# Performance work log

Measured on AMD Instinct MI355X. Metric: run time of the kernel, lower is better.

The kernel has to match this reference:

```python
import jax, jax.numpy as jnp
import numpy as np

B, S, D_IN, D_OUT, R = 8, 2048, 2048, 2048, 16

def setup_inputs() -> dict:
    key = jax.random.key(0)
    k = jax.random.split(key, 5)
    scale_w = 1.0 / np.sqrt(D_IN)
    return {
        "x": jax.random.normal(k[0], (B, S, D_IN), dtype=jnp.float32),
        "A_params": jax.random.normal(k[1], (B, D_OUT, R), dtype=jnp.float32) * 0.02,
        "B_params": jax.random.normal(k[2], (B, R, D_IN), dtype=jnp.float32) * 0.02,
        "W": jax.random.normal(k[3], (D_OUT, D_IN), dtype=jnp.float32) * scale_w,
        "b": jax.random.normal(k[4], (D_OUT,), dtype=jnp.float32) * scale_w,
    }

def reference(x, A_params, B_params, W, b):
    # base: x @ W^T + b  -> [B, S, out]
    base_out = jnp.einsum("bsi,oi->bso", x, W) + b
    # intermediate = x @ B^T -> [B, S, r]
    intermediate = jnp.einsum("bsi,bri->bsr", x, B_params)
    # adaptation = intermediate @ A^T -> [B, S, out]
    adaptation = jnp.einsum("bsr,bor->bso", intermediate, A_params)
    return base_out + adaptation
```

## Files before the change

### kernel.cpp

```cpp
#include <hip/hip_runtime.h>
#include <cstdint>
#include <cstddef>

typedef __attribute__((ext_vector_type(4))) float  floatx4;
typedef __attribute__((ext_vector_type(8))) __bf16 bf16x8;
typedef __attribute__((ext_vector_type(8))) unsigned short u16x8;

#define M_TOT 16384
#define N_TOT 2048
#define K_TOT 2048
#define NBATCH 8
#define RLORA 16
#define NT 32

__device__ __forceinline__ unsigned short f32_to_bf16(float f) {
  unsigned u = __float_as_uint(f);
  u += 0x7fffu + ((u >> 16) & 1u);
  return (unsigned short)(u >> 16);
}

__device__ __forceinline__ u16x8 cvt8(const float4& a, const float4& b) {
  u16x8 o;
  o[0] = f32_to_bf16(a.x); o[1] = f32_to_bf16(a.y);
  o[2] = f32_to_bf16(a.z); o[3] = f32_to_bf16(a.w);
  o[4] = f32_to_bf16(b.x); o[5] = f32_to_bf16(b.y);
  o[6] = f32_to_bf16(b.z); o[7] = f32_to_bf16(b.w);
  return o;
}

#define GLOAD_LDS16(gp, lp)                                                        \
  __builtin_amdgcn_global_load_lds((__attribute__((address_space(1))) void*)(void*)(gp), \
                                   (__attribute__((address_space(3))) void*)(void*)(lp), \
                                   16, 0, 0)

template<int V> struct IC { static constexpr int value = V; };

__global__ void k_convert_small(const float* __restrict__ W, const float* __restrict__ Ap,
                                unsigned short* __restrict__ wbf, unsigned short* __restrict__ abf) {
  int b = blockIdx.x;
  if (b < 2048) {
    int i = b * 256 + threadIdx.x;
    const float4* p = (const float4*)W + (size_t)i * 2;
    *(u16x8*)(wbf + (size_t)i * 8) = cvt8(p[0], p[1]);
  } else {
    int row = (b - 2048) * 256 + threadIdx.x;
    const float4* p = (const float4*)(Ap + (size_t)row * RLORA);
    u16x8 lo = cvt8(p[0], p[1]), hi2 = cvt8(p[2], p[3]), z = {0,0,0,0,0,0,0,0};
    u16x8* dst = (u16x8*)(abf + (size_t)row * 32);
    dst[0] = lo; dst[1] = hi2; dst[2] = z; dst[3] = z;
  }
}

__global__ __launch_bounds__(256) void k_xinter(const float* __restrict__ x,
                                                const float* __restrict__ Bp,
                                                unsigned short* __restrict__ xbf,
                                                unsigned short* __restrict__ interbf) {
  const int tid  = threadIdx.x;
  const int lane = tid & 63;
  const int wv   = tid >> 6;
  const int l15  = lane & 15;
  const int hi   = lane >> 4;
  const int m0   = blockIdx.x * 16;
  const int bb   = m0 >> 11;

  floatx4 acc = {0.f, 0.f, 0.f, 0.f};
  const float* bpb = Bp + (size_t)bb * (RLORA * K_TOT);
  const size_t xrow = (size_t)(m0 + l15) * K_TOT;
  const size_t brow = (size_t)l15 * K_TOT;
  const int kb0 = wv * 512;
  for (int kb = kb0; kb < kb0 + 512; kb += 32) {
    const float* xp = x + xrow + kb + hi * 8;
    u16x8 ao = cvt8(*(const float4*)xp, *(const float4*)(xp + 4));
    *(u16x8*)(xbf + xrow + kb + hi * 8) = ao;
    const float* bpp = bpb + brow + kb + hi * 8;
    u16x8 bo = cvt8(*(const float4*)bpp, *(const float4*)(bpp + 4));
    acc = __builtin_amdgcn_mfma_f32_16x16x32_bf16(*(bf16x8*)&ao, *(bf16x8*)&bo, acc, 0, 0, 0);
  }

  __shared__ floatx4 red[4][64];
  red[wv][lane] = acc;
  __syncthreads();
  if (wv == 0) {
    floatx4 s = red[0][lane] + red[1][lane] + red[2][lane] + red[3][lane];
    #pragma unroll
    for (int j = 0; j < 4; ++j) {
      int m = m0 + hi * 4 + j;
      interbf[(size_t)m * 32 + l15] = f32_to_bf16(s[j]);
      interbf[(size_t)m * 32 + 16 + l15] = 0;
    }
  }
}

#define STAGE_A(bufi, h, tt) do {                                                      \
  GLOAD_LDS16(Ag + (h)*262144 + (tt)*64 + gOff0, AsB + ((bufi)*2+(h))*16384 + ldsB0);  \
  GLOAD_LDS16(Ag + (h)*262144 + (tt)*64 + gOff1, AsB + ((bufi)*2+(h))*16384 + ldsB1);  \
} while(0)
#define STAGE_B(bufi, h, tt) do {                                                      \
  GLOAD_LDS16(Bg + (h)*262144 + (tt)*64 + gOff0, BsB + ((bufi)*2+(h))*16384 + ldsB0);  \
  GLOAD_LDS16(Bg + (h)*262144 + (tt)*64 + gOff1, BsB + ((bufi)*2+(h))*16384 + ldsB1);  \
} while(0)
#define RDA_(B2, q, mi, ks) (*(const bf16x8*)(AsB + (B2)*32768 + aBase + (q)*4096 + (mi)*2048 + koff[ks]))
#define RDB_(B2, ni, ks)    (*(const bf16x8*)(BsB + (B2)*32768 + bBase + (ni)*2048 + koff[ks]))
#define BAR() __builtin_amdgcn_s_barrier()

__global__ __launch_bounds__(512, 2) void k_gemm(const unsigned short* __restrict__ xbf,
                                                 const unsigned short* __restrict__ wbf,
                                                 const unsigned short* __restrict__ interbf,
                                                 const unsigned short* __restrict__ abf,
                                                 const float* __restrict__ bias,
                                                 float* __restrict__ out) {
  __shared__ unsigned short As[2][2][8192];
  __shared__ unsigned short Bs[2][2][8192];
  const int tid  = threadIdx.x;
  const int lane = tid & 63;
  const int wid  = tid >> 6;
  const int wm   = wid >> 2;
  const int wn   = wid & 3;
  const int l15  = lane & 15;
  const int hi   = lane >> 4;
  const int swz  = l15 & 7;

  int bid  = blockIdx.x;
  int swzb = ((bid & 7) << 6) | (bid >> 3);
  const int mt = swzb >> 3;
  const int nt = swzb & 7;
  const int mrow0 = mt << 8;
  const int ncol0 = nt << 8;
  const int bb = mrow0 >> 11;

  const int m0 = mrow0 + wm * 128;
  const int n0 = ncol0 + wn * 64;

  const unsigned short* Ag = xbf + (size_t)mrow0 * K_TOT;
  const unsigned short* Bg = wbf + (size_t)ncol0 * K_TOT;
  char* AsB = (char*)As;
  char* BsB = (char*)Bs;

  const int r0    = tid >> 3;
  const int k80   = (tid & 7) ^ (r0 & 7);
  const int gOff0 = r0 * K_TOT + k80 * 8;
  const int gOff1 = gOff0 + 64 * K_TOT;
  const int ldsB0 = wid * 1024;
  const int ldsB1 = 8192 + wid * 1024;

  const int aBase = wm * 16384 + l15 * 128;
  const int bBase = (wn >> 1) * 16384 + (wn & 1) * 8192 + l15 * 128;
  int koff[2];
  koff[0] = ((0 * 4 + hi) ^ swz) * 16;
  koff[1] = ((1 * 4 + hi) ^ swz) * 16;

  floatx4 acc[8][4];
  bf16x8 bfr[4][2];
  bf16x8 af[2][2];

  {
    bf16x8 la[8], lb[4];
    #pragma unroll
    for (int mi = 0; mi < 8; ++mi)
      la[mi] = *(const bf16x8*)(interbf + (size_t)(m0 + mi * 16 + l15) * 32 + hi * 8);
    #pragma unroll
    for (int ni = 0; ni < 4; ++ni)
      lb[ni] = *(const bf16x8*)(abf + ((size_t)bb * N_TOT + n0 + ni * 16 + l15) * 32 + hi * 8);

    STAGE_A(0, 0, 0); STAGE_A(0, 1, 0); STAGE_B(0, 0, 0); STAGE_B(0, 1, 0);
    STAGE_B(1, 0, 1); STAGE_B(1, 1, 1);

    floatx4 z = {0.f, 0.f, 0.f, 0.f};
    #pragma unroll
    for (int mi = 0; mi < 8; ++mi)
      #pragma unroll
      for (int ni = 0; ni < 4; ++ni)
        acc[mi][ni] = __builtin_amdgcn_mfma_f32_16x16x32_bf16(la[mi], lb[ni], z, 0, 0, 0);
  }
  asm volatile("s_waitcnt vmcnt(4)" ::: "memory");
  BAR();

  auto tile_step = [&](int t, auto bufc, auto sac, auto sbc, auto vmc) {
    constexpr int BUF = decltype(bufc)::value;
    constexpr int SA  = decltype(sac)::value;
    constexpr int SB  = decltype(sbc)::value;
    constexpr int VM  = decltype(vmc)::value;

    #pragma unroll
    for (int ni = 0; ni < 4; ++ni) { bfr[ni][0] = RDB_(BUF, ni, 0); bfr[ni][1] = RDB_(BUF, ni, 1); }
    #pragma unroll
    for (int mi = 0; mi < 2; ++mi) { af[mi][0] = RDA_(BUF, 0, mi, 0); af[mi][1] = RDA_(BUF, 0, mi, 1); }
    if constexpr (SA) STAGE_A(BUF ^ 1, 0, t + 1);
    BAR();
    __builtin_amdgcn_s_setprio(1);
    #pragma unroll
    for (int mi = 0; mi < 2; ++mi)
      #pragma unroll
      for (int ni = 0; ni < 4; ++ni) {
        acc[mi][ni] = __builtin_amdgcn_mfma_f32_16x16x32_bf16(af[mi][0], bfr[ni][0], acc[mi][ni], 0, 0, 0);
        acc[mi][ni] = __builtin_amdgcn_mfma_f32_16x16x32_bf16(af[mi][1], bfr[ni][1], acc[mi][ni], 0, 0, 0);
      }
    __builtin_amdgcn_s_setprio(0);
    BAR();

    #pragma unroll
    for (int mi = 0; mi < 2; ++mi) { af[mi][0] = RDA_(BUF, 1, mi, 0); af[mi][1] = RDA_(BUF, 1, mi, 1); }
    if constexpr (SA) STAGE_A(BUF ^ 1, 1, t + 1);
    BAR();
    __builtin_amdgcn_s_setprio(1);
    #pragma unroll
    for (int mi = 0; mi < 2; ++mi)
      #pragma unroll
      for (int ni = 0; ni < 4; ++ni) {
        acc[2+mi][ni] = __builtin_amdgcn_mfma_f32_16x16x32_bf16(af[mi][0], bfr[ni][0], acc[2+mi][ni], 0, 0, 0);
        acc[2+mi][ni] = __builtin_amdgcn_mfma_f32_16x16x32_bf16(af[mi][1], bfr[ni][1], acc[2+mi][ni], 0, 0, 0);
      }
    __builtin_amdgcn_s_setprio(0);
    BAR();

    #pragma unroll
    for (int mi = 0; mi < 2; ++mi) { af[mi][0] = RDA_(BUF, 2, mi, 0); af[mi][1] = RDA_(BUF, 2, mi, 1); }
    if constexpr (SB) STAGE_B(BUF, 0, t + 2);
    BAR();
    __builtin_amdgcn_s_setprio(1);
    #pragma unroll
    for (int mi = 0; mi < 2; ++mi)
      #pragma unroll
      for (int ni = 0; ni < 4; ++ni) {
        acc[4+mi][ni] = __builtin_amdgcn_mfma_f32_16x16x32_bf16(af[mi][0], bfr[ni][0], acc[4+mi][ni], 0, 0, 0);
        acc[4+mi][ni] = __builtin_amdgcn_mfma_f32_16x16x32_bf16(af[mi][1], bfr[ni][1], acc[4+mi][ni], 0, 0, 0);
      }
    __builtin_amdgcn_s_setprio(0);
    BAR();

    #pragma unroll
    for (int mi = 0; mi < 2; ++mi) { af[mi][0] = RDA_(BUF, 3, mi, 0); af[mi][1] = RDA_(BUF, 3, mi, 1); }
    if constexpr (SB) STAGE_B(BUF, 1, t + 2);
    BAR();
    __builtin_amdgcn_s_setprio(1);
    #pragma unroll
    for (int mi = 0; mi < 2; ++mi)
      #pragma unroll
      for (int ni = 0; ni < 4; ++ni) {
        acc[6+mi][ni] = __builtin_amdgcn_mfma_f32_16x16x32_bf16(af[mi][0], bfr[ni][0], acc[6+mi][ni], 0, 0, 0);
        acc[6+mi][ni] = __builtin_amdgcn_mfma_f32_16x16x32_bf16(af[mi][1], bfr[ni][1], acc[6+mi][ni], 0, 0, 0);
      }
    __builtin_amdgcn_s_setprio(0);
    if constexpr (VM == 4)      asm volatile("s_waitcnt vmcnt(4)" ::: "memory");
    else if constexpr (VM == 0) asm volatile("s_waitcnt vmcnt(0)" ::: "memory");
    BAR();
  };

  for (int t = 0; t < NT - 2; t += 2) {
    tile_step(t,     IC<0>{}, IC<1>{}, IC<1>{}, IC<4>{});
    tile_step(t + 1, IC<1>{}, IC<1>{}, IC<1>{}, IC<4>{});
  }
  tile_step(NT - 2, IC<0>{}, IC<1>{}, IC<0>{}, IC<0>{});
  tile_step(NT - 1, IC<1>{}, IC<0>{}, IC<0>{}, IC<-1>{});

  #pragma unroll
  for (int ni = 0; ni < 4; ++ni) {
    int col = n0 + ni * 16 + l15;
    float bv = bias[col];
    #pragma unroll
    for (int mi = 0; mi < 8; ++mi) {
      int r = m0 + mi * 16 + hi * 4;
      #pragma unroll
      for (int j = 0; j < 4; ++j)
        out[(size_t)(r + j) * N_TOT + col] = acc[mi][ni][j] + bv;
    }
  }
}

extern "C" void kernel_launch(void* const* d_in, const int* in_sizes, int n_in,
                              void* d_out, int out_size, void* d_ws, size_t ws_size,
                              hipStream_t stream) {
  const float* x    = (const float*)d_in[0];
  const float* Ap   = (const float*)d_in[1];
  const float* Bp   = (const float*)d_in[2];
  const float* W    = (const float*)d_in[3];
  const float* bias = (const float*)d_in[4];
  float* out = (float*)d_out;

  char* ws = (char*)d_ws;
  unsigned short* xbf     = (unsigned short*)(ws);
  unsigned short* wbf     = (unsigned short*)(ws + 67108864);
  unsigned short* abf     = (unsigned short*)(ws + 67108864 + 8388608);
  unsigned short* interbf = (unsigned short*)(ws + 67108864 + 8388608 + 1048576);

  k_convert_small<<<dim3(2112), dim3(256), 0, stream>>>(W, Ap, wbf, abf);
  k_xinter<<<dim3(1024), dim3(256), 0, stream>>>(x, Bp, xbf, interbf);
  k_gemm<<<dim3(512), dim3(512), 0, stream>>>(xbf, wbf, interbf, abf, bias, out);
}
```

Before: 192.6 us.

## Switch GEMM to 32x32x16 MFMA tiles and merge prep kernels into one launch

The main GEMM now issues 32x32x16 bf16 MFMA instructions instead of 16x16x32, with new accumulator layout, LDS read offsets and epilogue row mapping. Fewer, larger MFMAs per wave should cut instruction issue and LDS fragment reads per flop. The two conversion kernels are fused into one launch, and the LoRA rank buffers drop their zero padding from 32 to 16 columns. The cost is heavier register use for the 16-wide accumulators and a riskier fragment and output mapping.

```diff
diff --git a/kernel.cpp b/kernel.cpp
--- a/kernel.cpp
+++ b/kernel.cpp
@@ -2,9 +2,10 @@
 #include <cstdint>
 #include <cstddef>
 
-typedef __attribute__((ext_vector_type(4))) float  floatx4;
-typedef __attribute__((ext_vector_type(8))) __bf16 bf16x8;
-typedef __attribute__((ext_vector_type(8))) unsigned short u16x8;
+typedef __attribute__((ext_vector_type(4)))  float  floatx4;
+typedef __attribute__((ext_vector_type(16))) float  f32x16;
+typedef __attribute__((ext_vector_type(8)))  __bf16 bf16x8;
+typedef __attribute__((ext_vector_type(8)))  unsigned short u16x8;
 
 #define M_TOT 16384
 #define N_TOT 2048
@@ -35,32 +36,32 @@
 
 template<int V> struct IC { static constexpr int value = V; };
 
-__global__ void k_convert_small(const float* __restrict__ W, const float* __restrict__ Ap,
-                                unsigned short* __restrict__ wbf, unsigned short* __restrict__ abf) {
-  int b = blockIdx.x;
+__global__ __launch_bounds__(256) void k_prep(const float* __restrict__ W, const float* __restrict__ Ap,
+                                              const float* __restrict__ x, const float* __restrict__ Bp,
+                                              unsigned short* __restrict__ wbf, unsigned short* __restrict__ abf,
+                                              unsigned short* __restrict__ xbf, unsigned short* __restrict__ interbf) {
+  __shared__ floatx4 red[4][64];
+  const int b = blockIdx.x;
+  const int tid = threadIdx.x;
   if (b < 2048) {
-    int i = b * 256 + threadIdx.x;
+    int i = b * 256 + tid;
     const float4* p = (const float4*)W + (size_t)i * 2;
     *(u16x8*)(wbf + (size_t)i * 8) = cvt8(p[0], p[1]);
-  } else {
-    int row = (b - 2048) * 256 + threadIdx.x;
+    return;
+  }
+  if (b < 2112) {
+    int row = (b - 2048) * 256 + tid;
     const float4* p = (const float4*)(Ap + (size_t)row * RLORA);
-    u16x8 lo = cvt8(p[0], p[1]), hi2 = cvt8(p[2], p[3]), z = {0,0,0,0,0,0,0,0};
-    u16x8* dst = (u16x8*)(abf + (size_t)row * 32);
-    dst[0] = lo; dst[1] = hi2; dst[2] = z; dst[3] = z;
-  }
-}
-
-__global__ __launch_bounds__(256) void k_xinter(const float* __restrict__ x,
-                                                const float* __restrict__ Bp,
-                                                unsigned short* __restrict__ xbf,
-                                                unsigned short* __restrict__ interbf) {
-  const int tid  = threadIdx.x;
+    u16x8* dst = (u16x8*)(abf + (size_t)row * RLORA);
+    dst[0] = cvt8(p[0], p[1]);
+    dst[1] = cvt8(p[2], p[3]);
+    return;
+  }
   const int lane = tid & 63;
   const int wv   = tid >> 6;
   const int l15  = lane & 15;
   const int hi   = lane >> 4;
-  const int m0   = blockIdx.x * 16;
+  const int m0   = (b - 2112) * 16;
   const int bb   = m0 >> 11;
 
   floatx4 acc = {0.f, 0.f, 0.f, 0.f};
@@ -76,8 +77,6 @@
     u16x8 bo = cvt8(*(const float4*)bpp, *(const float4*)(bpp + 4));
     acc = __builtin_amdgcn_mfma_f32_16x16x32_bf16(*(bf16x8*)&ao, *(bf16x8*)&bo, acc, 0, 0, 0);
   }
-
-  __shared__ floatx4 red[4][64];
   red[wv][lane] = acc;
   __syncthreads();
   if (wv == 0) {
@@ -85,8 +84,7 @@
     #pragma unroll
     for (int j = 0; j < 4; ++j) {
       int m = m0 + hi * 4 + j;
-      interbf[(size_t)m * 32 + l15] = f32_to_bf16(s[j]);
-      interbf[(size_t)m * 32 + 16 + l15] = 0;
+      interbf[(size_t)m * RLORA + l15] = f32_to_bf16(s[j]);
     }
   }
 }
@@ -99,8 +97,8 @@
   GLOAD_LDS16(Bg + (h)*262144 + (tt)*64 + gOff0, BsB + ((bufi)*2+(h))*16384 + ldsB0);  \
   GLOAD_LDS16(Bg + (h)*262144 + (tt)*64 + gOff1, BsB + ((bufi)*2+(h))*16384 + ldsB1);  \
 } while(0)
-#define RDA_(B2, q, mi, ks) (*(const bf16x8*)(AsB + (B2)*32768 + aBase + (q)*4096 + (mi)*2048 + koff[ks]))
-#define RDB_(B2, ni, ks)    (*(const bf16x8*)(BsB + (B2)*32768 + bBase + (ni)*2048 + koff[ks]))
+#define RDA_(B2, mt, ks) (*(const bf16x8*)(AsB + (B2)*32768 + aBase + (mt)*4096 + koff[ks]))
+#define RDB_(B2, nt, ks) (*(const bf16x8*)(BsB + (B2)*32768 + bBase + (nt)*4096 + koff[ks]))
 #define BAR() __builtin_amdgcn_s_barrier()
 
 __global__ __launch_bounds__(512, 2) void k_gemm(const unsigned short* __restrict__ xbf,
@@ -116,16 +114,15 @@
   const int wid  = tid >> 6;
   const int wm   = wid >> 2;
   const int wn   = wid & 3;
-  const int l15  = lane & 15;
-  const int hi   = lane >> 4;
-  const int swz  = l15 & 7;
+  const int l31  = lane & 31;
+  const int g    = lane >> 5;
 
   int bid  = blockIdx.x;
   int swzb = ((bid & 7) << 6) | (bid >> 3);
-  const int mt = swzb >> 3;
-  const int nt = swzb & 7;
-  const int mrow0 = mt << 8;
-  const int ncol0 = nt << 8;
+  const int mt_ = swzb >> 3;
+  const int nt_ = swzb & 7;
+  const int mrow0 = mt_ << 8;
+  const int ncol0 = nt_ << 8;
   const int bb = mrow0 >> 11;
 
   const int m0 = mrow0 + wm * 128;
@@ -143,34 +140,34 @@
   const int ldsB0 = wid * 1024;
   const int ldsB1 = 8192 + wid * 1024;
 
-  const int aBase = wm * 16384 + l15 * 128;
-  const int bBase = (wn >> 1) * 16384 + (wn & 1) * 8192 + l15 * 128;
-  int koff[2];
-  koff[0] = ((0 * 4 + hi) ^ swz) * 16;
-  koff[1] = ((1 * 4 + hi) ^ swz) * 16;
-
-  floatx4 acc[8][4];
-  bf16x8 bfr[4][2];
-  bf16x8 af[2][2];
+  const int aBase = wm * 16384 + l31 * 128;
+  const int bBase = (wn >> 1) * 16384 + (wn & 1) * 8192 + l31 * 128;
+  int koff[4];
+  #pragma unroll
+  for (int ks = 0; ks < 4; ++ks) koff[ks] = ((ks * 2 + g) ^ (l31 & 7)) * 16;
+
+  f32x16 acc[4][2];
+  bf16x8 bfr[2][4];
+  bf16x8 af[4];
 
   {
-    bf16x8 la[8], lb[4];
-    #pragma unroll
-    for (int mi = 0; mi < 8; ++mi)
-      la[mi] = *(const bf16x8*)(interbf + (size_t)(m0 + mi * 16 + l15) * 32 + hi * 8);
-    #pragma unroll
-    for (int ni = 0; ni < 4; ++ni)
-      lb[ni] = *(const bf16x8*)(abf + ((size_t)bb * N_TOT + n0 + ni * 16 + l15) * 32 + hi * 8);
+    bf16x8 la[4], lb[2];
+    #pragma unroll
+    for (int mt = 0; mt < 4; ++mt)
+      la[mt] = *(const bf16x8*)(interbf + (size_t)(m0 + mt * 32 + l31) * RLORA + g * 8);
+    #pragma unroll
+    for (int nt = 0; nt < 2; ++nt)
+      lb[nt] = *(const bf16x8*)(abf + ((size_t)bb * N_TOT + n0 + nt * 32 + l31) * RLORA + g * 8);
 
     STAGE_A(0, 0, 0); STAGE_A(0, 1, 0); STAGE_B(0, 0, 0); STAGE_B(0, 1, 0);
     STAGE_B(1, 0, 1); STAGE_B(1, 1, 1);
 
-    floatx4 z = {0.f, 0.f, 0.f, 0.f};
-    #pragma unroll
-    for (int mi = 0; mi < 8; ++mi)
-      #pragma unroll
-      for (int ni = 0; ni < 4; ++ni)
-        acc[mi][ni] = __builtin_amdgcn_mfma_f32_16x16x32_bf16(la[mi], lb[ni], z, 0, 0, 0);
+    f32x16 z = {0.f};
+    #pragma unroll
+    for (int mt = 0; mt < 4; ++mt)
+      #pragma unroll
+      for (int nt = 0; nt < 2; ++nt)
+        acc[mt][nt] = __builtin_amdgcn_mfma_f32_32x32x16_bf16(la[mt], lb[nt], z, 0, 0, 0);
   }
   asm volatile("s_waitcnt vmcnt(4)" ::: "memory");
   BAR();
@@ -182,64 +179,58 @@
     constexpr int VM  = decltype(vmc)::value;
 
     #pragma unroll
-    for (int ni = 0; ni < 4; ++ni) { bfr[ni][0] = RDB_(BUF, ni, 0); bfr[ni][1] = RDB_(BUF, ni, 1); }
-    #pragma unroll
-    for (int mi = 0; mi < 2; ++mi) { af[mi][0] = RDA_(BUF, 0, mi, 0); af[mi][1] = RDA_(BUF, 0, mi, 1); }
+    for (int nt = 0; nt < 2; ++nt)
+      #pragma unroll
+      for (int ks = 0; ks < 4; ++ks) bfr[nt][ks] = RDB_(BUF, nt, ks);
+    #pragma unroll
+    for (int ks = 0; ks < 4; ++ks) af[ks] = RDA_(BUF, 0, ks);
     if constexpr (SA) STAGE_A(BUF ^ 1, 0, t + 1);
     BAR();
     __builtin_amdgcn_s_setprio(1);
     #pragma unroll
-    for (int mi = 0; mi < 2; ++mi)
-      #pragma unroll
-      for (int ni = 0; ni < 4; ++ni) {
-        acc[mi][ni] = __builtin_amdgcn_mfma_f32_16x16x32_bf16(af[mi][0], bfr[ni][0], acc[mi][ni], 0, 0, 0);
-        acc[mi][ni] = __builtin_amdgcn_mfma_f32_16x16x32_bf16(af[mi][1], bfr[ni][1], acc[mi][ni], 0, 0, 0);
-      }
-    __builtin_amdgcn_s_setprio(0);
-    BAR();
-
-    #pragma unroll
-    for (int mi = 0; mi < 2; ++mi) { af[mi][0] = RDA_(BUF, 1, mi, 0); af[mi][1] = RDA_(BUF, 1, mi, 1); }
+    for (int ks = 0; ks < 4; ++ks)
+      #pragma unroll
+      for (int nt = 0; nt < 2; ++nt)
+        acc[0][nt] = __builtin_amdgcn_mfma_f32_32x32x16_bf16(af[ks], bfr[nt][ks], acc[0][nt], 0, 0, 0);
+    __builtin_amdgcn_s_setprio(0);
+    BAR();
+
+    #pragma unroll
+    for (int ks = 0; ks < 4; ++ks) af[ks] = RDA_(BUF, 1, ks);
     if constexpr (SA) STAGE_A(BUF ^ 1, 1, t + 1);
     BAR();
     __builtin_amdgcn_s_setprio(1);
     #pragma unroll
-    for (int mi = 0; mi < 2; ++mi)
-      #pragma unroll
-      for (int ni = 0; ni < 4; ++ni) {
-        acc[2+mi][ni] = __builtin_amdgcn_mfma_f32_16x16x32_bf16(af[mi][0], bfr[ni][0], acc[2+mi][ni], 0, 0, 0);
-        acc[2+mi][ni] = __builtin_amdgcn_mfma_f32_16x16x32_bf16(af[mi][1], bfr[ni][1], acc[2+mi][ni], 0, 0, 0);
-      }
-    __builtin_amdgcn_s_setprio(0);
-    BAR();
-
-    #pragma unroll
-    for (int mi = 0; mi < 2; ++mi) { af[mi][0] = RDA_(BUF, 2, mi, 0); af[mi][1] = RDA_(BUF, 2, mi, 1); }
+    for (int ks = 0; ks < 4; ++ks)
+      #pragma unroll
+      for (int nt = 0; nt < 2; ++nt)
+        acc[1][nt] = __builtin_amdgcn_mfma_f32_32x32x16_bf16(af[ks], bfr[nt][ks], acc[1][nt], 0, 0, 0);
+    __builtin_amdgcn_s_setprio(0);
+    BAR();
+
+    #pragma unroll
+    for (int ks = 0; ks < 4; ++ks) af[ks] = RDA_(BUF, 2, ks);
     if constexpr (SB) STAGE_B(BUF, 0, t + 2);
     BAR();
     __builtin_amdgcn_s_setprio(1);
     #pragma unroll
-    for (int mi = 0; mi < 2; ++mi)
-      #pragma unroll
-      for (int ni = 0; ni < 4; ++ni) {
-        acc[4+mi][ni] = __builtin_amdgcn_mfma_f32_16x16x32_bf16(af[mi][0], bfr[ni][0], acc[4+mi][ni], 0, 0, 0);
-        acc[4+mi][ni] = __builtin_amdgcn_mfma_f32_16x16x32_bf16(af[mi][1], bfr[ni][1], acc[4+mi][ni], 0, 0, 0);
-      }
-    __builtin_amdgcn_s_setprio(0);
-    BAR();
-
-    #pragma unroll
-    for (int mi = 0; mi < 2; ++mi) { af[mi][0] = RDA_(BUF, 3, mi, 0); af[mi][1] = RDA_(BUF, 3, mi, 1); }
+    for (int ks = 0; ks < 4; ++ks)
+      #pragma unroll
+      for (int nt = 0; nt < 2; ++nt)
+        acc[2][nt] = __builtin_amdgcn_mfma_f32_32x32x16_bf16(af[ks], bfr[nt][ks], acc[2][nt], 0, 0, 0);
+    __builtin_amdgcn_s_setprio(0);
+    BAR();
+
+    #pragma unroll
+    for (int ks = 0; ks < 4; ++ks) af[ks] = RDA_(BUF, 3, ks);
     if constexpr (SB) STAGE_B(BUF, 1, t + 2);
     BAR();
     __builtin_amdgcn_s_setprio(1);
     #pragma unroll
-    for (int mi = 0; mi < 2; ++mi)
-      #pragma unroll
-      for (int ni = 0; ni < 4; ++ni) {
-        acc[6+mi][ni] = __builtin_amdgcn_mfma_f32_16x16x32_bf16(af[mi][0], bfr[ni][0], acc[6+mi][ni], 0, 0, 0);
-        acc[6+mi][ni] = __builtin_amdgcn_mfma_f32_16x16x32_bf16(af[mi][1], bfr[ni][1], acc[6+mi][ni], 0, 0, 0);
-      }
+    for (int ks = 0; ks < 4; ++ks)
+      #pragma unroll
+      for (int nt = 0; nt < 2; ++nt)
+        acc[3][nt] = __builtin_amdgcn_mfma_f32_32x32x16_bf16(af[ks], bfr[nt][ks], acc[3][nt], 0, 0, 0);
     __builtin_amdgcn_s_setprio(0);
     if constexpr (VM == 4)      asm volatile("s_waitcnt vmcnt(4)" ::: "memory");
     else if constexpr (VM == 0) asm volatile("s_waitcnt vmcnt(0)" ::: "memory");
@@ -254,15 +245,16 @@
   tile_step(NT - 1, IC<1>{}, IC<0>{}, IC<0>{}, IC<-1>{});
 
   #pragma unroll
-  for (int ni = 0; ni < 4; ++ni) {
-    int col = n0 + ni * 16 + l15;
+  for (int nt = 0; nt < 2; ++nt) {
+    int col = n0 + nt * 32 + l31;
     float bv = bias[col];
     #pragma unroll
-    for (int mi = 0; mi < 8; ++mi) {
-      int r = m0 + mi * 16 + hi * 4;
-      #pragma unroll
-      for (int j = 0; j < 4; ++j)
-        out[(size_t)(r + j) * N_TOT + col] = acc[mi][ni][j] + bv;
+    for (int mt = 0; mt < 4; ++mt) {
+      #pragma unroll
+      for (int reg = 0; reg < 16; ++reg) {
+        int row = m0 + mt * 32 + (reg & 3) + 8 * (reg >> 2) + 4 * g;
+        out[(size_t)row * N_TOT + col] = acc[mt][nt][reg] + bv;
+      }
     }
   }
 }
@@ -280,10 +272,9 @@
   char* ws = (char*)d_ws;
   unsigned short* xbf     = (unsigned short*)(ws);
   unsigned short* wbf     = (unsigned short*)(ws + 67108864);
-  unsigned short* abf     = (unsigned short*)(ws + 67108864 + 8388608);
-  unsigned short* interbf = (unsigned short*)(ws + 67108864 + 8388608 + 1048576);
-
-  k_convert_small<<<dim3(2112), dim3(256), 0, stream>>>(W, Ap, wbf, abf);
-  k_xinter<<<dim3(1024), dim3(256), 0, stream>>>(x, Bp, xbf, interbf);
+  unsigned short* abf     = (unsigned short*)(ws + 75497472);
+  unsigned short* interbf = (unsigned short*)(ws + 76021760);
+
+  k_prep<<<dim3(3136), dim3(256), 0, stream>>>(W, Ap, x, Bp, wbf, abf, xbf, interbf);
   k_gemm<<<dim3(512), dim3(512), 0, stream>>>(xbf, wbf, interbf, abf, bias, out);
 }
```

Measured after the change: 233.5 us. +21.2%, slower.
